# Optimization experiments

Measured on AMD Instinct MI355X. Metric: run time of the kernel, lower is better.

The kernel has to match this reference:

```python
import jax, jax.numpy as jnp
import numpy as np

N, D, E, NCLASS, NLAYERS = 50000, 32, 1600000, 40, 4
DT = 1.0
SCALE = 1.0 / np.sqrt(D)


def _transformer_conv(X, src, dst, Wq, bq, Wk, bk):
    # PyG TransformerConv, heads=1, lin_value=Identity, root_weight=False
    q = X @ Wq + bq                       # [N, D]
    k = X @ Wk + bk                       # [N, D]
    logits = jnp.sum(q[dst] * k[src], axis=-1) * SCALE   # [E]
    # numerically-stable scatter softmax over edges grouped by dst
    m = jax.lax.stop_gradient(jax.ops.segment_max(logits, dst, num_segments=N))
    e = jnp.exp(logits - m[dst])
    s = jax.ops.segment_sum(e, dst, num_segments=N)
    alpha = e / s[dst]                    # [E]
    # weighted scatter-sum aggregation of source features
    return jax.ops.segment_sum(alpha[:, None] * X[src], dst, num_segments=N)


def setup_inputs() -> dict:
    key = jax.random.key(0)
    ks = jax.random.split(key, 8)
    x = jax.random.normal(ks[0], (N, D), dtype=jnp.float32)
    edge_index = jax.random.randint(ks[1], (2, E), 0, N, dtype=jnp.int32)
    g = 1.0 / np.sqrt(D)
    Wq = jax.random.normal(ks[2], (D, D), dtype=jnp.float32) * g
    bq = jnp.zeros((D,), dtype=jnp.float32)
    Wk = jax.random.normal(ks[3], (D, D), dtype=jnp.float32) * g
    bk = jnp.zeros((D,), dtype=jnp.float32)
    Wr = jax.random.normal(ks[4], (D, NCLASS), dtype=jnp.float32) * g
    br = jnp.zeros((NCLASS,), dtype=jnp.float32)
    return {"x": x, "edge_index": edge_index, "Wq": Wq, "bq": bq,
            "Wk": Wk, "bk": bk, "Wr": Wr, "br": br}


def reference(x, edge_index, Wq, bq, Wk, bk, Wr, br):
    src, dst = edge_index[0], edge_index[1]   # PyG: row=source j, col=target i
    X = x                                      # emb is Identity; dropout=0 (eval)
    xs = [X]
    for _ in range(NLAYERS):                   # Euler ODE steps, fixed small count
        X = X + DT * (_transformer_conv(X, src, dst, Wq, bq, Wk, bk) - X)
        xs.append(X)
    out = X @ Wr + br                          # [N, NCLASS]
    X_all = jnp.stack(xs, axis=1)              # [N, NLAYERS+1, D]
    return (out, X_all)
```

## Files before the change

### kernel.cpp

```cpp
#include <hip/hip_runtime.h>
#include <hip/hip_fp16.h>
#include <math.h>

#define NN 50000
#define DD 32
#define EE 1600000
#define NCLS 40
#define NLAY 4
#define SCALE_C 0.17677669529663687f
#define EXP2SC  0.2550348710334252f
#define XSTRIDE (DD * (NLAY + 1))

#define NPB 128
#define NB  391
#define CAP 4608
#define TILE 8192
#define NBLK_SC 196
#define NBLK_PREP 782

typedef _Float16 f16x2 __attribute__((ext_vector_type(2)));
typedef unsigned int uint;
typedef unsigned short ushort;


__device__ __forceinline__ float fdot2(uint a, uint b, float c) {
#if __has_builtin(__builtin_amdgcn_fdot2)
    return __builtin_amdgcn_fdot2(__builtin_bit_cast(f16x2, a),
                                  __builtin_bit_cast(f16x2, b), c, false);
#else
    float2 af = __half22float2(__builtin_bit_cast(__half2, a));
    float2 bf = __half22float2(__builtin_bit_cast(__half2, b));
    return c + af.x * bf.x + af.y * bf.y;
#endif
}

__device__ __forceinline__ __half2 h2shfl_xor(__half2 v, int off) {
    return __builtin_bit_cast(__half2, __shfl_xor(__builtin_bit_cast(uint, v), off));
}

__global__ __launch_bounds__(256) void g_build(
    const int* __restrict__ src, const int* __restrict__ dst,
    int* __restrict__ bcur, int* __restrict__ packed,
    const float* __restrict__ x,
    const float* __restrict__ Wq, const float* __restrict__ bq,
    const float* __restrict__ Wk, const float* __restrict__ bk,
    const float* __restrict__ Wr,
    float* __restrict__ xall, __half* __restrict__ q16, __half* __restrict__ kx,
    uint* __restrict__ W16p)
{
    int b = blockIdx.x, t = threadIdx.x;
    if (b < NBLK_SC) {
        __shared__ int lhist[NB], gbase[NB], lcur[NB];
        for (int i = t; i < NB; i += 256) lhist[i] = 0;
        __syncthreads();
        int base = b * TILE;
        int es[32], eb[32];
#pragma unroll
        for (int j = 0; j < 32; ++j) {
            int e = base + j * 256 + t;
            if (e < EE) {
                int sv = src[e], dv = dst[e];
                es[j] = sv | ((dv & (NPB - 1)) << 16);
                eb[j] = dv >> 7;
                atomicAdd(&lhist[eb[j]], 1);
            } else eb[j] = -1;
        }
        __syncthreads();
        for (int i = t; i < NB; i += 256) {
            int c = lhist[i];
            gbase[i] = (c > 0) ? atomicAdd(&bcur[i], c) : 0;
            lcur[i] = 0;
        }
        __syncthreads();
#pragma unroll
        for (int j = 0; j < 32; ++j) {
            if (eb[j] >= 0) {
                int r = atomicAdd(&lcur[eb[j]], 1);
                packed[eb[j] * CAP + gbase[eb[j]] + r] = es[j];
            }
        }
    } else if (b < NBLK_SC + NBLK_PREP) {
        __shared__ float sWq[DD * DD], sWk[DD * DD], sbq[DD], sbk[DD];
        for (int i = t; i < DD * DD; i += 256) { sWq[i] = Wq[i]; sWk[i] = Wk[i]; }
        if (t < DD) { sbq[t] = bq[t]; sbk[t] = bk[t]; }
        __syncthreads();
        int b2 = b - NBLK_SC;
#pragma unroll
        for (int rep = 0; rep < 8; ++rep) {
            int tt = (b2 * 8 + rep) * 256 + t;
            if (tt >= NN * DD) break;
            int n = tt >> 5, j = tt & 31;
            const float* xr = x + n * DD;
            float aq = sbq[j], ak = sbk[j];
#pragma unroll
            for (int i = 0; i < DD; ++i) {
                float xv = xr[i];
                aq += xv * sWq[i * DD + j];
                ak += xv * sWk[i * DD + j];
            }
            float xv = xr[j];
            xall[n * XSTRIDE + j] = xv;
            q16[tt] = __float2half(aq);
            kx[n * 64 + j]      = __float2half(ak);
            kx[n * 64 + 32 + j] = __float2half(xv);
        }
    } else {
        for (int t2 = t; t2 < 1664; t2 += 256) {
            __half2 h;
            if (t2 < 1024) {
                int side = t2 >> 9, rest = t2 & 511, i = rest >> 5, j = rest & 31;
                const float* W = side ? Wk : Wq;
                h.x = __float2half(W[(2 * i) * DD + j]);
                h.y = __float2half(W[(2 * i + 1) * DD + j]);
            } else {
                int idx = t2 - 1024, i = idx / NCLS, c = idx % NCLS;
                h.x = __float2half(Wr[(2 * i) * NCLS + c]);
                h.y = __float2half(Wr[(2 * i + 1) * NCLS + c]);
            }
            W16p[t2] = __builtin_bit_cast(uint, h);
        }
    }
}

__global__ __launch_bounds__(256) void g_bfinal(
    const int* __restrict__ bcur, const int* __restrict__ packed,
    int* __restrict__ rowstart, int* __restrict__ degg,
    ushort* __restrict__ csr_src)
{
    __shared__ int ldeg[NPB], lpre[NPB], lc[NPB];
    int b = blockIdx.x, t = threadIdx.x;
    int cnt = min(bcur[b], CAP);
    int node0 = b << 7;
    int nn = min(NPB, NN - node0);
    if (t < NPB) ldeg[t] = 0;
    __syncthreads();
    const int* pk = packed + b * CAP;
    for (int i = t; i < cnt; i += 256) atomicAdd(&ldeg[pk[i] >> 16], 1);
    __syncthreads();
    if (t < NPB) lpre[t] = ldeg[t];
    __syncthreads();
    for (int off = 1; off < NPB; off <<= 1) {
        int v = 0;
        if (t < NPB && t >= off) v = lpre[t - off];
        __syncthreads();
        if (t < NPB) lpre[t] += v;
        __syncthreads();
    }
    int csrbase = b * CAP;
    if (t < nn) {
        int ex = lpre[t] - ldeg[t];
        rowstart[node0 + t] = csrbase + ex;
        degg[node0 + t] = ldeg[t];
        lc[t] = csrbase + ex;
    }
    __syncthreads();
    for (int i = t; i < cnt; i += 256) {
        int p = pk[i];
        int pos = atomicAdd(&lc[p >> 16], 1);
        csr_src[pos] = (ushort)(p & 0xFFFF);
    }
}

template<int DO_QK, int DO_OUT>
__global__ __launch_bounds__(256) void g_node(
    const int* __restrict__ rowstart, const int* __restrict__ degg,
    const ushort* __restrict__ csr_src,
    const __half* __restrict__ q16, const uint* __restrict__ kx,
    float* __restrict__ Xnext,
    __half* __restrict__ q16n, uint* __restrict__ kxn,
    const uint* __restrict__ W16p,
    const float* __restrict__ bq, const float* __restrict__ bk,
    const float* __restrict__ br, float* __restrict__ outp)
{
    __shared__ uint sX[4][2][16];
    int wv   = threadIdx.x >> 6;
    int lane = threadIdx.x & 63;
    int h  = lane >> 5;
    int l5 = lane & 31;
    int g  = l5 >> 2;
    int j  = lane & 3;
    int n = blockIdx.x * 8 + wv * 2 + h;
    int base = rowstart[n];
    int deg  = degg[n];

    uint4 qq = ((const uint4*)(q16 + n * DD))[j];

    float s_part = 0.0f;
    __half2 zero2 = __float2half2_rn(0.0f);
    __half2 a01 = zero2, a23 = zero2, a45 = zero2, a67 = zero2;
    int dm1 = deg - 1;

#pragma unroll 2
    for (int i0 = 0; i0 < deg; i0 += 8) {
        int i = i0 + g;
        bool valid = i < deg;
        int sn = (int)csr_src[base + min(i, dm1)];
        const uint4* row = (const uint4*)(kx + sn * 32);
        uint4 kk = row[j];
        uint4 xx = row[4 + j];
        float dotp = fdot2(kk.w, qq.w, fdot2(kk.z, qq.z,
                     fdot2(kk.y, qq.y, fdot2(kk.x, qq.x, 0.0f))));
        dotp += __shfl_xor(dotp, 1);
        dotp += __shfl_xor(dotp, 2);
        dotp = valid ? dotp : -INFINITY;
        float w = exp2f(dotp * EXP2SC);
        s_part += w;
        __half2 wh2 = __float2half2_rn(w);
        a01 = __hfma2(wh2, __builtin_bit_cast(__half2, xx.x), a01);
        a23 = __hfma2(wh2, __builtin_bit_cast(__half2, xx.y), a23);
        a45 = __hfma2(wh2, __builtin_bit_cast(__half2, xx.z), a45);
        a67 = __hfma2(wh2, __builtin_bit_cast(__half2, xx.w), a67);
    }
#pragma unroll
    for (int off = 4; off <= 16; off <<= 1) {
        s_part += __shfl_xor(s_part, off);
        a01 = __hadd2(a01, h2shfl_xor(a01, off));
        a23 = __hadd2(a23, h2shfl_xor(a23, off));
        a45 = __hadd2(a45, h2shfl_xor(a45, off));
        a67 = __hadd2(a67, h2shfl_xor(a67, off));
    }
    float inv = (deg > 0) ? 1.0f / s_part : 0.0f;
    __half2 inv2 = __float2half2_rn(inv);
    __half2 o01 = __hmul2(a01, inv2), o23 = __hmul2(a23, inv2);
    __half2 o45 = __hmul2(a45, inv2), o67 = __hmul2(a67, inv2);

    if (g == 0) {
        float2 f01 = __half22float2(o01), f23 = __half22float2(o23);
        float2 f45 = __half22float2(o45), f67 = __half22float2(o67);
        float4 lo; lo.x = f01.x; lo.y = f01.y; lo.z = f23.x; lo.w = f23.y;
        float4 hi; hi.x = f45.x; hi.y = f45.y; hi.z = f67.x; hi.w = f67.y;
        float* xo = Xnext + n * XSTRIDE + 8 * j;
        *(float4*)xo = lo;
        *(float4*)(xo + 4) = hi;
        uint4 st;
        st.x = __builtin_bit_cast(uint, o01); st.y = __builtin_bit_cast(uint, o23);
        st.z = __builtin_bit_cast(uint, o45); st.w = __builtin_bit_cast(uint, o67);
        if (DO_QK) ((uint4*)(kxn + n * 32))[4 + j] = st;
        sX[wv][h][4 * j + 0] = st.x; sX[wv][h][4 * j + 1] = st.y;
        sX[wv][h][4 * j + 2] = st.z; sX[wv][h][4 * j + 3] = st.w;
    }
    if (DO_QK) {
        int j2 = lane & 31, side = lane >> 5;
        const uint* Wcol = W16p + side * 512;
        float bb = side ? bk[j2] : bq[j2];
#pragma unroll
        for (int hh = 0; hh < 2; ++hh) {
            int nh = blockIdx.x * 8 + wv * 2 + hh;
            float acc = bb;
#pragma unroll
            for (int i = 0; i < 16; ++i)
                acc = fdot2(Wcol[i * 32 + j2], sX[wv][hh][i], acc);
            __half hv = __float2half(acc);
            if (side == 0) q16n[nh * DD + j2] = hv;
            else ((__half*)kxn)[nh * 64 + j2] = hv;
        }
    }
    if (DO_OUT) {
        const uint* Wr16 = W16p + 1024;
        int c = lane;
#pragma unroll
        for (int hh = 0; hh < 2; ++hh) {
            int nh = blockIdx.x * 8 + wv * 2 + hh;
            if (c < NCLS) {
                float acc = br[c];
#pragma unroll
                for (int i = 0; i < 16; ++i)
                    acc = fdot2(Wr16[i * NCLS + c], sX[wv][hh][i], acc);
                outp[nh * NCLS + c] = acc;
            }
        }
    }
}

extern "C" void kernel_launch(void* const* d_in, const int* in_sizes, int n_in,
                              void* d_out, int out_size, void* d_ws, size_t ws_size,
                              hipStream_t stream) {
    const float* x  = (const float*)d_in[0];
    const int*   ei = (const int*)d_in[1];
    const int*   src = ei;
    const int*   dst = ei + EE;
    const float* Wq = (const float*)d_in[2];
    const float* bq = (const float*)d_in[3];
    const float* Wk = (const float*)d_in[4];
    const float* bk = (const float*)d_in[5];
    const float* Wr = (const float*)d_in[6];
    const float* br = (const float*)d_in[7];

    float* out  = (float*)d_out;
    float* xall = out + (size_t)NN * NCLS;

    char* wsp = (char*)d_ws;
    __half* q16A = (__half*)wsp;                       wsp += sizeof(__half) * NN * DD;
    __half* q16B = (__half*)wsp;                       wsp += sizeof(__half) * NN * DD;
    uint*   kxA  = (uint*)wsp;                         wsp += sizeof(uint) * NN * 32;
    uint*   kxB  = (uint*)wsp;                         wsp += sizeof(uint) * NN * 32;
    uint*   W16p = (uint*)wsp;                         wsp += sizeof(uint) * 2048;
    int* bcur     = (int*)wsp;                         wsp += sizeof(int) * NB;
    int* rowstart = (int*)wsp;                         wsp += sizeof(int) * NN;
    int* degg     = (int*)wsp;                         wsp += sizeof(int) * NN;
    int* packed   = (int*)wsp;                         wsp += sizeof(int) * NB * CAP;
    ushort* csr_src = (ushort*)wsp;                    wsp += sizeof(ushort) * NB * CAP;

    const int B = 256;

    hipMemsetAsync(bcur, 0, sizeof(int) * NB, stream);
    g_build<<<NBLK_SC + NBLK_PREP + 1, B, 0, stream>>>(
        src, dst, bcur, packed, x, Wq, bq, Wk, bk, Wr, xall, q16A, (__half*)kxA, W16p);
    g_bfinal<<<NB, B, 0, stream>>>(bcur, packed, rowstart, degg, csr_src);

    for (int l = 0; l < NLAY; ++l) {
        float* Xnxt = xall + (l + 1) * DD;
        __half* qc = (l & 1) ? q16B : q16A;
        __half* qn = (l & 1) ? q16A : q16B;
        uint*   kc = (l & 1) ? kxB : kxA;
        uint*   kn = (l & 1) ? kxA : kxB;
        if (l < NLAY - 1)
            g_node<1, 0><<<NN / 8, B, 0, stream>>>(rowstart, degg, csr_src, qc, kc,
                                                   Xnxt, qn, kn, W16p, bq, bk, br, out);
        else
            g_node<0, 1><<<NN / 8, B, 0, stream>>>(rowstart, degg, csr_src, qc, kc,
                                                   Xnxt, qn, kn, W16p, bq, bk, br, out);
    }
}
```

Baseline: 165.0 us.

## Sort nodes by degree within buckets and prefetch next neighbor index

g_bfinal now counting-sorts the nodes of each 128-node bucket by in-degree and writes a permutation. g_node uses that permutation so the two half-waves and nearby waves handle nodes of similar degree, which is meant to cut loop divergence where one half-wave idles while the other finishes a longer neighbor list. The csr_src index for the next iteration is also loaded one step ahead to hide that dependent load. The cost is an extra perm lookup per node, less regular Xnext/q/k write addresses, and a longer bfinal kernel.

```diff
diff --git a/kernel.cpp b/kernel.cpp
--- a/kernel.cpp
+++ b/kernel.cpp
@@ -125,14 +125,16 @@
 __global__ __launch_bounds__(256) void g_bfinal(
     const int* __restrict__ bcur, const int* __restrict__ packed,
     int* __restrict__ rowstart, int* __restrict__ degg,
-    ushort* __restrict__ csr_src)
+    ushort* __restrict__ csr_src, int* __restrict__ perm)
 {
     __shared__ int ldeg[NPB], lpre[NPB], lc[NPB];
+    __shared__ int dh[256], dps[256], dcur[256];
     int b = blockIdx.x, t = threadIdx.x;
     int cnt = min(bcur[b], CAP);
     int node0 = b << 7;
     int nn = min(NPB, NN - node0);
     if (t < NPB) ldeg[t] = 0;
+    dh[t] = 0;
     __syncthreads();
     const int* pk = packed + b * CAP;
     for (int i = t; i < cnt; i += 256) atomicAdd(&ldeg[pk[i] >> 16], 1);
@@ -159,12 +161,28 @@
         int pos = atomicAdd(&lc[p >> 16], 1);
         csr_src[pos] = (ushort)(p & 0xFFFF);
     }
+    if (t < nn) atomicAdd(&dh[min(ldeg[t], 255)], 1);
+    __syncthreads();
+    dps[t] = dh[t];
+    __syncthreads();
+    for (int off = 1; off < 256; off <<= 1) {
+        int v = (t >= off) ? dps[t - off] : 0;
+        __syncthreads();
+        dps[t] += v;
+        __syncthreads();
+    }
+    dcur[t] = dps[t] - dh[t];
+    __syncthreads();
+    if (t < nn) {
+        int p = atomicAdd(&dcur[min(ldeg[t], 255)], 1);
+        perm[node0 + p] = node0 + t;
+    }
 }
 
 template<int DO_QK, int DO_OUT>
 __global__ __launch_bounds__(256) void g_node(
     const int* __restrict__ rowstart, const int* __restrict__ degg,
-    const ushort* __restrict__ csr_src,
+    const ushort* __restrict__ csr_src, const int* __restrict__ perm,
     const __half* __restrict__ q16, const uint* __restrict__ kx,
     float* __restrict__ Xnext,
     __half* __restrict__ q16n, uint* __restrict__ kxn,
@@ -179,23 +197,26 @@
     int l5 = lane & 31;
     int g  = l5 >> 2;
     int j  = lane & 3;
-    int n = blockIdx.x * 8 + wv * 2 + h;
-    int base = rowstart[n];
-    int deg  = degg[n];
-
-    uint4 qq = ((const uint4*)(q16 + n * DD))[j];
+    int gid = blockIdx.x * 8 + wv * 2 + h;
+    int nd = perm[gid];
+    int base = rowstart[nd];
+    int deg  = degg[nd];
+
+    uint4 qq = ((const uint4*)(q16 + nd * DD))[j];
 
     float s_part = 0.0f;
     __half2 zero2 = __float2half2_rn(0.0f);
     __half2 a01 = zero2, a23 = zero2, a45 = zero2, a67 = zero2;
-    int dm1 = deg - 1;
-
+    int dmax = max(deg - 1, 0);
+
+    int sn = (int)csr_src[base + min(g, dmax)];
 #pragma unroll 2
     for (int i0 = 0; i0 < deg; i0 += 8) {
         int i = i0 + g;
         bool valid = i < deg;
-        int sn = (int)csr_src[base + min(i, dm1)];
-        const uint4* row = (const uint4*)(kx + sn * 32);
+        int cur = sn;
+        sn = (int)csr_src[base + min(i + 8, dmax)];
+        const uint4* row = (const uint4*)(kx + cur * 32);
         uint4 kk = row[j];
         uint4 xx = row[4 + j];
         float dotp = fdot2(kk.w, qq.w, fdot2(kk.z, qq.z,
@@ -229,13 +250,13 @@
         float2 f45 = __half22float2(o45), f67 = __half22float2(o67);
         float4 lo; lo.x = f01.x; lo.y = f01.y; lo.z = f23.x; lo.w = f23.y;
         float4 hi; hi.x = f45.x; hi.y = f45.y; hi.z = f67.x; hi.w = f67.y;
-        float* xo = Xnext + n * XSTRIDE + 8 * j;
+        float* xo = Xnext + nd * XSTRIDE + 8 * j;
         *(float4*)xo = lo;
         *(float4*)(xo + 4) = hi;
         uint4 st;
         st.x = __builtin_bit_cast(uint, o01); st.y = __builtin_bit_cast(uint, o23);
         st.z = __builtin_bit_cast(uint, o45); st.w = __builtin_bit_cast(uint, o67);
-        if (DO_QK) ((uint4*)(kxn + n * 32))[4 + j] = st;
+        if (DO_QK) ((uint4*)(kxn + nd * 32))[4 + j] = st;
         sX[wv][h][4 * j + 0] = st.x; sX[wv][h][4 * j + 1] = st.y;
         sX[wv][h][4 * j + 2] = st.z; sX[wv][h][4 * j + 3] = st.w;
     }
@@ -245,7 +266,7 @@
         float bb = side ? bk[j2] : bq[j2];
 #pragma unroll
         for (int hh = 0; hh < 2; ++hh) {
-            int nh = blockIdx.x * 8 + wv * 2 + hh;
+            int nh = perm[blockIdx.x * 8 + wv * 2 + hh];
             float acc = bb;
 #pragma unroll
             for (int i = 0; i < 16; ++i)
@@ -260,7 +281,7 @@
         int c = lane;
 #pragma unroll
         for (int hh = 0; hh < 2; ++hh) {
-            int nh = blockIdx.x * 8 + wv * 2 + hh;
+            int nh = perm[blockIdx.x * 8 + wv * 2 + hh];
             if (c < NCLS) {
                 float acc = br[c];
 #pragma unroll
@@ -298,6 +319,7 @@
     int* bcur     = (int*)wsp;                         wsp += sizeof(int) * NB;
     int* rowstart = (int*)wsp;                         wsp += sizeof(int) * NN;
     int* degg     = (int*)wsp;                         wsp += sizeof(int) * NN;
+    int* perm     = (int*)wsp;                         wsp += sizeof(int) * NN;
     int* packed   = (int*)wsp;                         wsp += sizeof(int) * NB * CAP;
     ushort* csr_src = (ushort*)wsp;                    wsp += sizeof(ushort) * NB * CAP;
 
@@ -306,7 +328,7 @@
     hipMemsetAsync(bcur, 0, sizeof(int) * NB, stream);
     g_build<<<NBLK_SC + NBLK_PREP + 1, B, 0, stream>>>(
         src, dst, bcur, packed, x, Wq, bq, Wk, bk, Wr, xall, q16A, (__half*)kxA, W16p);
-    g_bfinal<<<NB, B, 0, stream>>>(bcur, packed, rowstart, degg, csr_src);
+    g_bfinal<<<NB, B, 0, stream>>>(bcur, packed, rowstart, degg, csr_src, perm);
 
     for (int l = 0; l < NLAY; ++l) {
         float* Xnxt = xall + (l + 1) * DD;
@@ -315,10 +337,10 @@
         uint*   kc = (l & 1) ? kxB : kxA;
         uint*   kn = (l & 1) ? kxA : kxB;
         if (l < NLAY - 1)
-            g_node<1, 0><<<NN / 8, B, 0, stream>>>(rowstart, degg, csr_src, qc, kc,
+            g_node<1, 0><<<NN / 8, B, 0, stream>>>(rowstart, degg, csr_src, perm, qc, kc,
                                                    Xnxt, qn, kn, W16p, bq, bk, br, out);
         else
-            g_node<0, 1><<<NN / 8, B, 0, stream>>>(rowstart, degg, csr_src, qc, kc,
+            g_node<0, 1><<<NN / 8, B, 0, stream>>>(rowstart, degg, csr_src, perm, qc, kc,
                                                    Xnxt, qn, kn, W16p, bq, bk, br, out);
     }
 }
```

New measurement: 183.5 us. +11.2%, slower.

## Stage bucketed edges in shared memory to coalesce packed global writes

Applied to the files above, without the earlier changes.

The edge-bucketing blocks now build a local histogram first, run a block-wide prefix scan, and scatter each packed edge into a bucket-sorted shared-memory staging buffer. They then write the staged edges to global memory in linear order, so consecutive threads store to contiguous runs within each bucket instead of scattering randomly. The cost is a second read of dst, a scan, and extra barriers in the build phase. Shared memory is unified into one buffer reused by the prep blocks. A small degree guard and a masking fix cover the extra bucket bits added to the packed word.

```diff
diff --git a/kernel.cpp b/kernel.cpp
--- a/kernel.cpp
+++ b/kernel.cpp
@@ -37,6 +37,14 @@
 __device__ __forceinline__ __half2 h2shfl_xor(__half2 v, int off) {
     return __builtin_bit_cast(__half2, __shfl_xor(__builtin_bit_cast(uint, v), off));
 }
+
+#define SM_STAGE 0
+#define SM_HIST  8192
+#define SM_SCX   (8192 + 392)
+#define SM_GB    (8192 + 2 * 392)
+#define SM_LC    (8192 + 3 * 392)
+#define SM_PS    (8192 + 4 * 392)
+#define SM_SIZE  (8192 + 4 * 392 + 256)
 
 __global__ __launch_bounds__(256) void g_build(
     const int* __restrict__ src, const int* __restrict__ dst,
@@ -48,39 +56,66 @@
     float* __restrict__ xall, __half* __restrict__ q16, __half* __restrict__ kx,
     uint* __restrict__ W16p)
 {
+    __shared__ uint smem[SM_SIZE];
     int b = blockIdx.x, t = threadIdx.x;
     if (b < NBLK_SC) {
-        __shared__ int lhist[NB], gbase[NB], lcur[NB];
-        for (int i = t; i < NB; i += 256) lhist[i] = 0;
+        int* hist  = (int*)(smem + SM_HIST);
+        int* scx   = (int*)(smem + SM_SCX);
+        int* gbase = (int*)(smem + SM_GB);
+        int* lcur  = (int*)(smem + SM_LC);
+        int* ps    = (int*)(smem + SM_PS);
+        uint* stage = smem + SM_STAGE;
+        for (int i = t; i < 392; i += 256) { hist[i] = 0; lcur[i] = 0; }
         __syncthreads();
         int base = b * TILE;
-        int es[32], eb[32];
+        int totalv = min(TILE, EE - base);
+#pragma unroll
+        for (int j = 0; j < 32; ++j) {
+            int e = base + j * 256 + t;
+            if (e < EE) atomicAdd(&hist[dst[e] >> 7], 1);
+        }
+        __syncthreads();
+        int h0 = (2 * t < 392)     ? hist[2 * t]     : 0;
+        int h1 = (2 * t + 1 < 392) ? hist[2 * t + 1] : 0;
+        ps[t] = h0 + h1;
+        __syncthreads();
+        for (int off = 1; off < 256; off <<= 1) {
+            int v = (t >= off) ? ps[t - off] : 0;
+            __syncthreads();
+            ps[t] += v;
+            __syncthreads();
+        }
+        int pex = ps[t] - (h0 + h1);
+        if (2 * t < 392)     scx[2 * t]     = pex;
+        if (2 * t + 1 < 392) scx[2 * t + 1] = pex + h0;
+        __syncthreads();
+        for (int i = t; i < NB; i += 256) {
+            int c = hist[i];
+            gbase[i] = (c > 0) ? atomicAdd(&bcur[i], c) : 0;
+        }
+        __syncthreads();
 #pragma unroll
         for (int j = 0; j < 32; ++j) {
             int e = base + j * 256 + t;
             if (e < EE) {
                 int sv = src[e], dv = dst[e];
-                es[j] = sv | ((dv & (NPB - 1)) << 16);
-                eb[j] = dv >> 7;
-                atomicAdd(&lhist[eb[j]], 1);
-            } else eb[j] = -1;
-        }
-        __syncthreads();
-        for (int i = t; i < NB; i += 256) {
-            int c = lhist[i];
-            gbase[i] = (c > 0) ? atomicAdd(&bcur[i], c) : 0;
-            lcur[i] = 0;
-        }
-        __syncthreads();
-#pragma unroll
-        for (int j = 0; j < 32; ++j) {
-            if (eb[j] >= 0) {
-                int r = atomicAdd(&lcur[eb[j]], 1);
-                packed[eb[j] * CAP + gbase[eb[j]] + r] = es[j];
+                int eb = dv >> 7;
+                int r = atomicAdd(&lcur[eb], 1);
+                stage[scx[eb] + r] = (uint)(sv | ((dv & (NPB - 1)) << 16) | ((uint)eb << 23));
             }
         }
+        __syncthreads();
+        for (int i = t; i < totalv; i += 256) {
+            uint v = stage[i];
+            int eb = (int)(v >> 23);
+            int pos = i - scx[eb];
+            packed[eb * CAP + gbase[eb] + pos] = (int)(v & 0x7FFFFF);
+        }
     } else if (b < NBLK_SC + NBLK_PREP) {
-        __shared__ float sWq[DD * DD], sWk[DD * DD], sbq[DD], sbk[DD];
+        float* sWq = (float*)smem;
+        float* sWk = (float*)smem + 1024;
+        float* sbq = (float*)smem + 2048;
+        float* sbk = (float*)smem + 2080;
         for (int i = t; i < DD * DD; i += 256) { sWq[i] = Wq[i]; sWk[i] = Wk[i]; }
         if (t < DD) { sbq[t] = bq[t]; sbk[t] = bk[t]; }
         __syncthreads();
@@ -135,7 +170,7 @@
     if (t < NPB) ldeg[t] = 0;
     __syncthreads();
     const int* pk = packed + b * CAP;
-    for (int i = t; i < cnt; i += 256) atomicAdd(&ldeg[pk[i] >> 16], 1);
+    for (int i = t; i < cnt; i += 256) atomicAdd(&ldeg[(pk[i] >> 16) & 127], 1);
     __syncthreads();
     if (t < NPB) lpre[t] = ldeg[t];
     __syncthreads();
@@ -156,7 +191,7 @@
     __syncthreads();
     for (int i = t; i < cnt; i += 256) {
         int p = pk[i];
-        int pos = atomicAdd(&lc[p >> 16], 1);
+        int pos = atomicAdd(&lc[(p >> 16) & 127], 1);
         csr_src[pos] = (ushort)(p & 0xFFFF);
     }
 }
@@ -188,7 +223,7 @@
     float s_part = 0.0f;
     __half2 zero2 = __float2half2_rn(0.0f);
     __half2 a01 = zero2, a23 = zero2, a45 = zero2, a67 = zero2;
-    int dm1 = deg - 1;
+    int dm1 = max(deg - 1, 0);
 
 #pragma unroll 2
     for (int i0 = 0; i0 < deg; i0 += 8) {
```

New measurement: 168.7 us. 1.02x slower.
